# Kernel optimization log

Measured on AMD Instinct MI355X. Metric: run time of the kernel, lower is better.

Reference implementation:

```python
import jax, jax.numpy as jnp
import numpy as np

N, DIN, DOUT = 8192, 256, 128
NEG_SLOPE = 0.01         # F.leaky_relu default
MASK_VAL = -9.0e15       # from the torch source


def setup_inputs() -> dict:
    key = jax.random.key(0)
    kx, kadj, kW, kbW, ka1, ka2, kba = jax.random.split(key, 7)
    x = jax.random.normal(kx, (N, DIN), dtype=jnp.float32)
    adj = jax.random.randint(kadj, (N, N), 0, 2, dtype=jnp.int32)
    # Linear W: input_dim -> output_dim
    W = jax.random.normal(kW, (DIN, DOUT), dtype=jnp.float32) * (1.0 / np.sqrt(DIN))
    bW = jax.random.normal(kbW, (DOUT,), dtype=jnp.float32) * 0.01
    # Linear a: 2*output_dim -> 1, split into the h_i part (a1) and h_j part (a2)
    a1 = jax.random.normal(ka1, (DOUT,), dtype=jnp.float32) * (1.0 / np.sqrt(2 * DOUT))
    a2 = jax.random.normal(ka2, (DOUT,), dtype=jnp.float32) * (1.0 / np.sqrt(2 * DOUT))
    ba = jax.random.normal(kba, (), dtype=jnp.float32) * 0.01
    return {"x": x, "adj": adj, "W": W, "bW": bW, "a1": a1, "a2": a2, "ba": ba}


def reference(x, adj, W, bW, a1, a2, ba):
    # h = W x + b  -> [N, DOUT]
    h = x @ W + bW
    # e[i,j] = leaky_relu(a . [h_i, h_j] + ba) = leaky_relu(a1.h_i + a2.h_j + ba)
    s_src = h @ a1            # [N]
    s_dst = h @ a2            # [N]
    e = s_src[:, None] + s_dst[None, :] + ba   # [N, N]
    e = jnp.where(e > 0, e, NEG_SLOPE * e)
    # mask non-edges, row softmax over neighbors j
    e = jnp.where(adj > 0, e, MASK_VAL)
    alpha = jax.nn.softmax(e, axis=1)          # [N, N]
    # dropout is identity in eval mode (dropout_rate=0)
    return alpha @ h                            # [N, DOUT]
```

## Files before the change

kernel.cpp:

```cpp
#include <hip/hip_runtime.h>
#include <hip/hip_bf16.h>


#define NN 8192
#define DIN 256
#define DOUT 128
#define LOG2E 1.4426950408889634f

typedef __attribute__((ext_vector_type(8))) short short8;
typedef __attribute__((ext_vector_type(4))) float floatx4;

__global__ void prep_wt(const float* __restrict__ W, __hip_bfloat16* __restrict__ WT) {
    int e = blockIdx.x * blockDim.x + threadIdx.x;
    if (e < DIN * DOUT) {
        int k = e >> 7;
        int d = e & 127;
        WT[d * DIN + k] = __float2bfloat16(W[e]);
    }
}

__global__ __launch_bounds__(256, 4) void gat_h(
    const float* __restrict__ x, const __hip_bfloat16* __restrict__ WT,
    const float* __restrict__ bW, const float* __restrict__ a1, const float* __restrict__ a2,
    __hip_bfloat16* __restrict__ hbB, float* __restrict__ s_src, float* __restrict__ s_dst) {
    int tid = threadIdx.x;
    int w = tid >> 6, lane = tid & 63;
    int lm = lane & 15, lq = lane >> 4;
    int i0 = blockIdx.x * 32;
    int r0 = (w >> 1) * 16;
    int c0 = (w & 1) * 64;

    __shared__ float s1s[32], s2s[32];
    if (tid < 32) { s1s[tid] = 0.f; s2s[tid] = 0.f; }
    __syncthreads();

    floatx4 acc[4] = {};
#pragma unroll
    for (int kk = 0; kk < DIN; kk += 32) {
        const float4* xp = (const float4*)&x[(size_t)(i0 + r0 + lm) * DIN + kk + lq * 8];
        float4 xa = xp[0], xb = xp[1];
        union { short8 v; __hip_bfloat16 h[8]; } af;
        af.h[0] = __float2bfloat16(xa.x); af.h[1] = __float2bfloat16(xa.y);
        af.h[2] = __float2bfloat16(xa.z); af.h[3] = __float2bfloat16(xa.w);
        af.h[4] = __float2bfloat16(xb.x); af.h[5] = __float2bfloat16(xb.y);
        af.h[6] = __float2bfloat16(xb.z); af.h[7] = __float2bfloat16(xb.w);
#pragma unroll
        for (int t = 0; t < 4; t++) {
            int d = c0 + 16 * t + lm;
            short8 bf = *(const short8*)&WT[(size_t)d * DIN + kk + lq * 8];
            acc[t] = __builtin_amdgcn_mfma_f32_16x16x32_bf16(af.v, bf, acc[t], 0, 0, 0);
        }
    }
    float s1[4] = {0.f, 0.f, 0.f, 0.f}, s2[4] = {0.f, 0.f, 0.f, 0.f};
#pragma unroll
    for (int t = 0; t < 4; t++) {
        int d = c0 + 16 * t + lm;
        int f = (c0 >> 4) + t;
        float A1 = a1[d], A2 = a2[d], B = bW[d];
#pragma unroll
        for (int r = 0; r < 4; r++) {
            int k = r0 + lq * 4 + r;
            float h = acc[t][r] + B;
            hbB[(size_t)blockIdx.x * 4096 + f * 512 + (k >> 3) * 128 + lm * 8 + (k & 7)] =
                __float2bfloat16(h);
            s1[r] += h * A1;
            s2[r] += h * A2;
        }
    }
#pragma unroll
    for (int r = 0; r < 4; r++) {
        for (int m = 1; m < 16; m <<= 1) {
            s1[r] += __shfl_xor(s1[r], m, 64);
            s2[r] += __shfl_xor(s2[r], m, 64);
        }
    }
    if (lm == 0) {
#pragma unroll
        for (int r = 0; r < 4; r++) {
            int row = r0 + lq * 4 + r;
            atomicAdd(&s1s[row], s1[r]);
            atomicAdd(&s2s[row], s2[r]);
        }
    }
    __syncthreads();
    if (tid < 32) {
        s_src[i0 + tid] = s1s[tid] * LOG2E;
        s_dst[i0 + tid] = s2s[tid] * LOG2E;
    }
}

template <int NJT>
__global__ void build_mask(const int* __restrict__ adj, unsigned char* __restrict__ mask) {
    size_t gid = (size_t)blockIdx.x * blockDim.x + threadIdx.x;
    const int4* a = (const int4*)(adj + gid * 8);
    int4 v0 = a[0], v1 = a[1];
    unsigned int b = 0;
    b |= (v0.x != 0) ? 1u : 0u;
    b |= (v0.y != 0) ? 2u : 0u;
    b |= (v0.z != 0) ? 4u : 0u;
    b |= (v0.w != 0) ? 8u : 0u;
    b |= (v1.x != 0) ? 16u : 0u;
    b |= (v1.y != 0) ? 32u : 0u;
    b |= (v1.z != 0) ? 64u : 0u;
    b |= (v1.w != 0) ? 128u : 0u;
    unsigned int g = (unsigned int)gid & (NJT * 4 - 1);
    size_t pos = (gid & ~(size_t)(NJT * 4 - 1)) | ((g & 3) * NJT + (g >> 2));
    mask[pos] = (unsigned char)b;
}

__device__ inline short8 make_pfrag(unsigned int cm, float ssi, float4 cd0, float4 cd1,
                                    floatx4* accd, const short8 ones) {
    float p[8];
    float e;
    e = ssi + cd0.x; e = fmaxf(e, 0.01f * e); p[0] = (cm & 1u)   ? __builtin_amdgcn_exp2f(e) : 0.f;
    e = ssi + cd0.y; e = fmaxf(e, 0.01f * e); p[1] = (cm & 2u)   ? __builtin_amdgcn_exp2f(e) : 0.f;
    e = ssi + cd0.z; e = fmaxf(e, 0.01f * e); p[2] = (cm & 4u)   ? __builtin_amdgcn_exp2f(e) : 0.f;
    e = ssi + cd0.w; e = fmaxf(e, 0.01f * e); p[3] = (cm & 8u)   ? __builtin_amdgcn_exp2f(e) : 0.f;
    e = ssi + cd1.x; e = fmaxf(e, 0.01f * e); p[4] = (cm & 16u)  ? __builtin_amdgcn_exp2f(e) : 0.f;
    e = ssi + cd1.y; e = fmaxf(e, 0.01f * e); p[5] = (cm & 32u)  ? __builtin_amdgcn_exp2f(e) : 0.f;
    e = ssi + cd1.z; e = fmaxf(e, 0.01f * e); p[6] = (cm & 64u)  ? __builtin_amdgcn_exp2f(e) : 0.f;
    e = ssi + cd1.w; e = fmaxf(e, 0.01f * e); p[7] = (cm & 128u) ? __builtin_amdgcn_exp2f(e) : 0.f;
    union { short8 v; __hip_bfloat162 q[4]; } af;
    af.q[0] = __float22bfloat162_rn(make_float2(p[0], p[1]));
    af.q[1] = __float22bfloat162_rn(make_float2(p[2], p[3]));
    af.q[2] = __float22bfloat162_rn(make_float2(p[4], p[5]));
    af.q[3] = __float22bfloat162_rn(make_float2(p[6], p[7]));
    *accd = __builtin_amdgcn_mfma_f32_16x16x32_bf16(af.v, ones, *accd, 0, 0, 0);
    return af.v;
}

template <int NJT>
__global__ __launch_bounds__(256, 3) void gat_attn(
    const unsigned char* __restrict__ mask, const float* __restrict__ s_src,
    const float* __restrict__ s_dst, const float* __restrict__ ba_p,
    const __hip_bfloat16* __restrict__ hbB,
    float* __restrict__ num, float* __restrict__ lpart) {
    int tid = threadIdx.x;
    int w = tid >> 6, lane = tid & 63;
    int lm = lane & 15, lq = lane >> 4;
    int b = blockIdx.x;
    int ib = b & 63;
    int jh = b >> 6;
    int i0 = ib * 128 + w * 32;
    int jb0 = jh * (NJT * 32);

    const unsigned char* mrow0 = mask + (size_t)(i0 + lm) * (NN / 8) + jh * (NJT * 4) + lq * NJT;
    const unsigned char* mrow1 = mrow0 + (size_t)16 * (NN / 8);
    union Mr { uint4 v[NJT / 16]; unsigned int u[NJT / 4]; };
    Mr mr0, mr1;
#pragma unroll
    for (int q = 0; q < NJT / 16; q++) {
        mr0.v[q] = ((const uint4*)mrow0)[q];
        mr1.v[q] = ((const uint4*)mrow1)[q];
    }

    float ba = ba_p[0] * LOG2E;
    float ssi0 = s_src[i0 + lm] + ba;
    float ssi1 = s_src[i0 + 16 + lm] + ba;
    const float* sd = s_dst + jb0 + lq * 8;
    const __hip_bfloat16* hb = hbB + ((size_t)(jh * NJT) * 8) * 512 + lane * 8;

    floatx4 acc0[8] = {}, acc1[8] = {};
    floatx4 accd0 = {}, accd1 = {};
    const short8 ones = { 0x3F80, 0x3F80, 0x3F80, 0x3F80, 0x3F80, 0x3F80, 0x3F80, 0x3F80 };

#pragma unroll
    for (int t = 0; t < NJT; t++) {
        unsigned int cm0 = (mr0.u[t >> 2] >> ((t & 3) * 8)) & 0xFFu;
        unsigned int cm1 = (mr1.u[t >> 2] >> ((t & 3) * 8)) & 0xFFu;
        float4 cd0 = *(const float4*)(sd + t * 32);
        float4 cd1 = *(const float4*)(sd + t * 32 + 4);
        short8 af0 = make_pfrag(cm0, ssi0, cd0, cd1, &accd0, ones);
        short8 af1 = make_pfrag(cm1, ssi1, cd0, cd1, &accd1, ones);

        const __hip_bfloat16* hbt = hb + (size_t)t * 8 * 512;
#pragma unroll
        for (int f = 0; f < 8; f++) {
            short8 bf = *(const short8*)(hbt + f * 512);
            acc0[f] = __builtin_amdgcn_mfma_f32_16x16x32_bf16(af0, bf, acc0[f], 0, 0, 0);
            acc1[f] = __builtin_amdgcn_mfma_f32_16x16x32_bf16(af1, bf, acc1[f], 0, 0, 0);
        }
    }

    float* nb = num + ((size_t)jh * NN + i0) * DOUT;
#pragma unroll
    for (int f = 0; f < 8; f++)
#pragma unroll
        for (int r = 0; r < 4; r++) {
            nb[(size_t)(lq * 4 + r) * DOUT + f * 16 + lm] = acc0[f][r];
            nb[(size_t)(16 + lq * 4 + r) * DOUT + f * 16 + lm] = acc1[f][r];
        }
    if (lm == 0) {
#pragma unroll
        for (int r = 0; r < 4; r++) {
            lpart[(size_t)jh * NN + i0 + lq * 4 + r] = accd0[r];
            lpart[(size_t)jh * NN + i0 + 16 + lq * 4 + r] = accd1[r];
        }
    }
}

__global__ void gat_combine(const float* __restrict__ num, const float* __restrict__ lpart,
                            float* __restrict__ out, int jsplit) {
    int gid = blockIdx.x * blockDim.x + threadIdx.x;
    int idx = gid * 4;
    int i = idx >> 7;
    float den = 0.f;
    for (int s = 0; s < jsplit; s++) den += lpart[(size_t)s * NN + i];
    float inv = 1.0f / den;
    float4 o = make_float4(0.f, 0.f, 0.f, 0.f);
    for (int s = 0; s < jsplit; s++) {
        float4 n = *(const float4*)&num[(size_t)s * NN * DOUT + idx];
        o.x += n.x; o.y += n.y; o.z += n.z; o.w += n.w;
    }
    o.x *= inv; o.y *= inv; o.z *= inv; o.w *= inv;
    *(float4*)&out[idx] = o;
}

extern "C" void kernel_launch(void* const* d_in, const int* in_sizes, int n_in,
                              void* d_out, int out_size, void* d_ws, size_t ws_size,
                              hipStream_t stream) {
    const float* x  = (const float*)d_in[0];
    const int* adj  = (const int*)d_in[1];
    const float* W  = (const float*)d_in[2];
    const float* bW = (const float*)d_in[3];
    const float* a1 = (const float*)d_in[4];
    const float* a2 = (const float*)d_in[5];
    const float* ba = (const float*)d_in[6];
    float* out = (float*)d_out;

    char* ws = (char*)d_ws;
    __hip_bfloat16* hbB  = (__hip_bfloat16*)ws;
    __hip_bfloat16* WT   = (__hip_bfloat16*)(ws + 2097152);
    float* s_src         = (float*)(ws + 2162688);
    float* s_dst         = (float*)(ws + 2195456);
    float* lpart         = (float*)(ws + 2228224);
    unsigned char* mask  = (unsigned char*)(ws + 2752512);
    float* num           = (float*)(ws + 11141120);

    int jsplit = (ws_size >= 11141120 + (size_t)16 * NN * DOUT * 4) ? 16 : 8;

    if (jsplit == 16) build_mask<16><<<32768, 256, 0, stream>>>(adj, mask);
    else              build_mask<32><<<32768, 256, 0, stream>>>(adj, mask);
    prep_wt<<<128, 256, 0, stream>>>(W, WT);
    gat_h<<<256, 256, 0, stream>>>(x, WT, bW, a1, a2, hbB, s_src, s_dst);
    if (jsplit == 16)
        gat_attn<16><<<1024, 256, 0, stream>>>(mask, s_src, s_dst, ba, hbB, num, lpart);
    else
        gat_attn<32><<<512, 256, 0, stream>>>(mask, s_src, s_dst, ba, hbB, num, lpart);
    gat_combine<<<1024, 256, 0, stream>>>(num, lpart, out, jsplit);
}
```

Measured before the change: 437.3 us.

## Stream adjacency directly into LDS in attention kernel, drop mask-build pass

Removes the separate build_mask kernel, which read the full int32 adjacency and wrote a bit mask. The attention kernel now streams adjacency tiles straight into LDS with global_load_lds in a double buffer and reads the int values to decide masking. This saves one full pass over the 256 MB adjacency plus a kernel launch. In exchange it adds a __syncthreads per tile and 32 KB of LDS per block, which may reduce occupancy.

```diff
diff --git a/kernel.cpp b/kernel.cpp
--- a/kernel.cpp
+++ b/kernel.cpp
@@ -9,6 +9,8 @@
 
 typedef __attribute__((ext_vector_type(8))) short short8;
 typedef __attribute__((ext_vector_type(4))) float floatx4;
+typedef __attribute__((address_space(3))) void lds_void;
+typedef __attribute__((address_space(1))) void gbl_void;
 
 __global__ void prep_wt(const float* __restrict__ W, __hip_bfloat16* __restrict__ WT) {
     int e = blockIdx.x * blockDim.x + threadIdx.x;
@@ -89,37 +91,18 @@
     }
 }
 
-template <int NJT>
-__global__ void build_mask(const int* __restrict__ adj, unsigned char* __restrict__ mask) {
-    size_t gid = (size_t)blockIdx.x * blockDim.x + threadIdx.x;
-    const int4* a = (const int4*)(adj + gid * 8);
-    int4 v0 = a[0], v1 = a[1];
-    unsigned int b = 0;
-    b |= (v0.x != 0) ? 1u : 0u;
-    b |= (v0.y != 0) ? 2u : 0u;
-    b |= (v0.z != 0) ? 4u : 0u;
-    b |= (v0.w != 0) ? 8u : 0u;
-    b |= (v1.x != 0) ? 16u : 0u;
-    b |= (v1.y != 0) ? 32u : 0u;
-    b |= (v1.z != 0) ? 64u : 0u;
-    b |= (v1.w != 0) ? 128u : 0u;
-    unsigned int g = (unsigned int)gid & (NJT * 4 - 1);
-    size_t pos = (gid & ~(size_t)(NJT * 4 - 1)) | ((g & 3) * NJT + (g >> 2));
-    mask[pos] = (unsigned char)b;
-}
-
-__device__ inline short8 make_pfrag(unsigned int cm, float ssi, float4 cd0, float4 cd1,
+__device__ inline short8 make_pfrag(int4 m0, int4 m1, float ssi, float4 cd0, float4 cd1,
                                     floatx4* accd, const short8 ones) {
     float p[8];
     float e;
-    e = ssi + cd0.x; e = fmaxf(e, 0.01f * e); p[0] = (cm & 1u)   ? __builtin_amdgcn_exp2f(e) : 0.f;
-    e = ssi + cd0.y; e = fmaxf(e, 0.01f * e); p[1] = (cm & 2u)   ? __builtin_amdgcn_exp2f(e) : 0.f;
-    e = ssi + cd0.z; e = fmaxf(e, 0.01f * e); p[2] = (cm & 4u)   ? __builtin_amdgcn_exp2f(e) : 0.f;
-    e = ssi + cd0.w; e = fmaxf(e, 0.01f * e); p[3] = (cm & 8u)   ? __builtin_amdgcn_exp2f(e) : 0.f;
-    e = ssi + cd1.x; e = fmaxf(e, 0.01f * e); p[4] = (cm & 16u)  ? __builtin_amdgcn_exp2f(e) : 0.f;
-    e = ssi + cd1.y; e = fmaxf(e, 0.01f * e); p[5] = (cm & 32u)  ? __builtin_amdgcn_exp2f(e) : 0.f;
-    e = ssi + cd1.z; e = fmaxf(e, 0.01f * e); p[6] = (cm & 64u)  ? __builtin_amdgcn_exp2f(e) : 0.f;
-    e = ssi + cd1.w; e = fmaxf(e, 0.01f * e); p[7] = (cm & 128u) ? __builtin_amdgcn_exp2f(e) : 0.f;
+    e = ssi + cd0.x; e = fmaxf(e, 0.01f * e); p[0] = m0.x ? __builtin_amdgcn_exp2f(e) : 0.f;
+    e = ssi + cd0.y; e = fmaxf(e, 0.01f * e); p[1] = m0.y ? __builtin_amdgcn_exp2f(e) : 0.f;
+    e = ssi + cd0.z; e = fmaxf(e, 0.01f * e); p[2] = m0.z ? __builtin_amdgcn_exp2f(e) : 0.f;
+    e = ssi + cd0.w; e = fmaxf(e, 0.01f * e); p[3] = m0.w ? __builtin_amdgcn_exp2f(e) : 0.f;
+    e = ssi + cd1.x; e = fmaxf(e, 0.01f * e); p[4] = m1.x ? __builtin_amdgcn_exp2f(e) : 0.f;
+    e = ssi + cd1.y; e = fmaxf(e, 0.01f * e); p[5] = m1.y ? __builtin_amdgcn_exp2f(e) : 0.f;
+    e = ssi + cd1.z; e = fmaxf(e, 0.01f * e); p[6] = m1.z ? __builtin_amdgcn_exp2f(e) : 0.f;
+    e = ssi + cd1.w; e = fmaxf(e, 0.01f * e); p[7] = m1.w ? __builtin_amdgcn_exp2f(e) : 0.f;
     union { short8 v; __hip_bfloat162 q[4]; } af;
     af.q[0] = __float22bfloat162_rn(make_float2(p[0], p[1]));
     af.q[1] = __float22bfloat162_rn(make_float2(p[2], p[3]));
@@ -131,10 +114,11 @@
 
 template <int NJT>
 __global__ __launch_bounds__(256, 3) void gat_attn(
-    const unsigned char* __restrict__ mask, const float* __restrict__ s_src,
+    const int* __restrict__ adj, const float* __restrict__ s_src,
     const float* __restrict__ s_dst, const float* __restrict__ ba_p,
     const __hip_bfloat16* __restrict__ hbB,
     float* __restrict__ num, float* __restrict__ lpart) {
+    __shared__ int stg[2][4][1024];
     int tid = threadIdx.x;
     int w = tid >> 6, lane = tid & 63;
     int lm = lane & 15, lq = lane >> 4;
@@ -144,15 +128,7 @@
     int i0 = ib * 128 + w * 32;
     int jb0 = jh * (NJT * 32);
 
-    const unsigned char* mrow0 = mask + (size_t)(i0 + lm) * (NN / 8) + jh * (NJT * 4) + lq * NJT;
-    const unsigned char* mrow1 = mrow0 + (size_t)16 * (NN / 8);
-    union Mr { uint4 v[NJT / 16]; unsigned int u[NJT / 4]; };
-    Mr mr0, mr1;
-#pragma unroll
-    for (int q = 0; q < NJT / 16; q++) {
-        mr0.v[q] = ((const uint4*)mrow0)[q];
-        mr1.v[q] = ((const uint4*)mrow1)[q];
-    }
+    const int* gstage = adj + (size_t)(i0 + (lane >> 3)) * NN + jb0 + (lane & 7) * 4;
 
     float ba = ba_p[0] * LOG2E;
     float ssi0 = s_src[i0 + lm] + ba;
@@ -165,13 +141,30 @@
     const short8 ones = { 0x3F80, 0x3F80, 0x3F80, 0x3F80, 0x3F80, 0x3F80, 0x3F80, 0x3F80 };
 
 #pragma unroll
+    for (int q = 0; q < 4; q++)
+        __builtin_amdgcn_global_load_lds(
+            (const gbl_void*)(gstage + (size_t)q * 8 * NN),
+            (lds_void*)&stg[0][w][q * 256 + lane * 4], 16, 0, 0);
+
+#pragma unroll
     for (int t = 0; t < NJT; t++) {
-        unsigned int cm0 = (mr0.u[t >> 2] >> ((t & 3) * 8)) & 0xFFu;
-        unsigned int cm1 = (mr1.u[t >> 2] >> ((t & 3) * 8)) & 0xFFu;
+        __syncthreads();
+        if (t + 1 < NJT) {
+#pragma unroll
+            for (int q = 0; q < 4; q++)
+                __builtin_amdgcn_global_load_lds(
+                    (const gbl_void*)(gstage + (t + 1) * 32 + (size_t)q * 8 * NN),
+                    (lds_void*)&stg[(t + 1) & 1][w][q * 256 + lane * 4], 16, 0, 0);
+        }
+        const int* sb = &stg[t & 1][w][0];
+        int4 a00 = *(const int4*)&sb[lm * 32 + lq * 8];
+        int4 a01 = *(const int4*)&sb[lm * 32 + lq * 8 + 4];
+        int4 a10 = *(const int4*)&sb[(16 + lm) * 32 + lq * 8];
+        int4 a11 = *(const int4*)&sb[(16 + lm) * 32 + lq * 8 + 4];
         float4 cd0 = *(const float4*)(sd + t * 32);
         float4 cd1 = *(const float4*)(sd + t * 32 + 4);
-        short8 af0 = make_pfrag(cm0, ssi0, cd0, cd1, &accd0, ones);
-        short8 af1 = make_pfrag(cm1, ssi1, cd0, cd1, &accd1, ones);
+        short8 af0 = make_pfrag(a00, a01, ssi0, cd0, cd1, &accd0, ones);
+        short8 af1 = make_pfrag(a10, a11, ssi1, cd0, cd1, &accd1, ones);
 
         const __hip_bfloat16* hbt = hb + (size_t)t * 8 * 512;
 #pragma unroll
@@ -234,18 +227,15 @@
     float* s_src         = (float*)(ws + 2162688);
     float* s_dst         = (float*)(ws + 2195456);
     float* lpart         = (float*)(ws + 2228224);
-    unsigned char* mask  = (unsigned char*)(ws + 2752512);
-    float* num           = (float*)(ws + 11141120);
-
-    int jsplit = (ws_size >= 11141120 + (size_t)16 * NN * DOUT * 4) ? 16 : 8;
-
-    if (jsplit == 16) build_mask<16><<<32768, 256, 0, stream>>>(adj, mask);
-    else              build_mask<32><<<32768, 256, 0, stream>>>(adj, mask);
+    float* num           = (float*)(ws + 2752512);
+
+    int jsplit = (ws_size >= 2752512 + (size_t)16 * NN * DOUT * 4) ? 16 : 8;
+
     prep_wt<<<128, 256, 0, stream>>>(W, WT);
     gat_h<<<256, 256, 0, stream>>>(x, WT, bW, a1, a2, hbB, s_src, s_dst);
     if (jsplit == 16)
-        gat_attn<16><<<1024, 256, 0, stream>>>(mask, s_src, s_dst, ba, hbB, num, lpart);
+        gat_attn<16><<<1024, 256, 0, stream>>>(adj, s_src, s_dst, ba, hbB, num, lpart);
     else
-        gat_attn<32><<<512, 256, 0, stream>>>(mask, s_src, s_dst, ba, hbB, num, lpart);
+        gat_attn<32><<<512, 256, 0, stream>>>(adj, s_src, s_dst, ba, hbB, num, lpart);
     gat_combine<<<1024, 256, 0, stream>>>(num, lpart, out, jsplit);
 }
```

Result: slower. 453.2 us (+3.7%).

## Fuse split-K combine into attention kernel with per-block shared-memory reduction

Applied to the files above, without the earlier changes.

Each block now handles 32 rows across all columns, with its four waves splitting the column range and reducing numerators and denominators through shared-memory atomics. The normalization is done in-kernel, which removes the partial num/lpart buffers and the separate combine kernel. This removes a large round trip of partial results through global memory. In exchange, the grid shrinks to 256 blocks at low occupancy, and each block streams all of h, which raises L2 traffic and reduces latency hiding.

```diff
diff --git a/kernel.cpp b/kernel.cpp
--- a/kernel.cpp
+++ b/kernel.cpp
@@ -89,7 +89,6 @@
     }
 }
 
-template <int NJT>
 __global__ void build_mask(const int* __restrict__ adj, unsigned char* __restrict__ mask) {
     size_t gid = (size_t)blockIdx.x * blockDim.x + threadIdx.x;
     const int4* a = (const int4*)(adj + gid * 8);
@@ -103,8 +102,8 @@
     b |= (v1.y != 0) ? 32u : 0u;
     b |= (v1.z != 0) ? 64u : 0u;
     b |= (v1.w != 0) ? 128u : 0u;
-    unsigned int g = (unsigned int)gid & (NJT * 4 - 1);
-    size_t pos = (gid & ~(size_t)(NJT * 4 - 1)) | ((g & 3) * NJT + (g >> 2));
+    unsigned int g = (unsigned int)gid & 255u;
+    size_t pos = (gid & ~(size_t)255) | ((g & 3u) * 64u + (g >> 2));
     mask[pos] = (unsigned char)b;
 }
 
@@ -129,27 +128,26 @@
     return af.v;
 }
 
-template <int NJT>
-__global__ __launch_bounds__(256, 3) void gat_attn(
+__global__ __launch_bounds__(256, 1) void gat_attn(
     const unsigned char* __restrict__ mask, const float* __restrict__ s_src,
     const float* __restrict__ s_dst, const float* __restrict__ ba_p,
-    const __hip_bfloat16* __restrict__ hbB,
-    float* __restrict__ num, float* __restrict__ lpart) {
+    const __hip_bfloat16* __restrict__ hbB, float* __restrict__ out) {
+    __shared__ float red[32][128];
+    __shared__ float den[32];
     int tid = threadIdx.x;
     int w = tid >> 6, lane = tid & 63;
     int lm = lane & 15, lq = lane >> 4;
-    int b = blockIdx.x;
-    int ib = b & 63;
-    int jh = b >> 6;
-    int i0 = ib * 128 + w * 32;
-    int jb0 = jh * (NJT * 32);
-
-    const unsigned char* mrow0 = mask + (size_t)(i0 + lm) * (NN / 8) + jh * (NJT * 4) + lq * NJT;
+    int i0 = blockIdx.x * 32;
+
+    for (int q = tid; q < 32 * 128; q += 256) ((float*)red)[q] = 0.f;
+    if (tid < 32) den[tid] = 0.f;
+
+    const unsigned char* mrow0 = mask + (size_t)(i0 + lm) * (NN / 8) + w * 256 + lq * 64;
     const unsigned char* mrow1 = mrow0 + (size_t)16 * (NN / 8);
-    union Mr { uint4 v[NJT / 16]; unsigned int u[NJT / 4]; };
+    union Mr { uint4 v[4]; unsigned int u[16]; };
     Mr mr0, mr1;
 #pragma unroll
-    for (int q = 0; q < NJT / 16; q++) {
+    for (int q = 0; q < 4; q++) {
         mr0.v[q] = ((const uint4*)mrow0)[q];
         mr1.v[q] = ((const uint4*)mrow1)[q];
     }
@@ -157,15 +155,17 @@
     float ba = ba_p[0] * LOG2E;
     float ssi0 = s_src[i0 + lm] + ba;
     float ssi1 = s_src[i0 + 16 + lm] + ba;
-    const float* sd = s_dst + jb0 + lq * 8;
-    const __hip_bfloat16* hb = hbB + ((size_t)(jh * NJT) * 8) * 512 + lane * 8;
+    const float* sd = s_dst + w * 2048 + lq * 8;
+    const __hip_bfloat16* hb = hbB + (size_t)(w * 64) * 4096 + lane * 8;
 
     floatx4 acc0[8] = {}, acc1[8] = {};
     floatx4 accd0 = {}, accd1 = {};
     const short8 ones = { 0x3F80, 0x3F80, 0x3F80, 0x3F80, 0x3F80, 0x3F80, 0x3F80, 0x3F80 };
 
-#pragma unroll
-    for (int t = 0; t < NJT; t++) {
+    __syncthreads();
+
+#pragma unroll 4
+    for (int t = 0; t < 64; t++) {
         unsigned int cm0 = (mr0.u[t >> 2] >> ((t & 3) * 8)) & 0xFFu;
         unsigned int cm1 = (mr1.u[t >> 2] >> ((t & 3) * 8)) & 0xFFu;
         float4 cd0 = *(const float4*)(sd + t * 32);
@@ -173,7 +173,7 @@
         short8 af0 = make_pfrag(cm0, ssi0, cd0, cd1, &accd0, ones);
         short8 af1 = make_pfrag(cm1, ssi1, cd0, cd1, &accd1, ones);
 
-        const __hip_bfloat16* hbt = hb + (size_t)t * 8 * 512;
+        const __hip_bfloat16* hbt = hb + (size_t)t * 4096;
 #pragma unroll
         for (int f = 0; f < 8; f++) {
             short8 bf = *(const short8*)(hbt + f * 512);
@@ -182,38 +182,31 @@
         }
     }
 
-    float* nb = num + ((size_t)jh * NN + i0) * DOUT;
 #pragma unroll
     for (int f = 0; f < 8; f++)
 #pragma unroll
         for (int r = 0; r < 4; r++) {
-            nb[(size_t)(lq * 4 + r) * DOUT + f * 16 + lm] = acc0[f][r];
-            nb[(size_t)(16 + lq * 4 + r) * DOUT + f * 16 + lm] = acc1[f][r];
+            atomicAdd(&red[lq * 4 + r][f * 16 + lm], acc0[f][r]);
+            atomicAdd(&red[16 + lq * 4 + r][f * 16 + lm], acc1[f][r]);
         }
     if (lm == 0) {
 #pragma unroll
         for (int r = 0; r < 4; r++) {
-            lpart[(size_t)jh * NN + i0 + lq * 4 + r] = accd0[r];
-            lpart[(size_t)jh * NN + i0 + 16 + lq * 4 + r] = accd1[r];
-        }
-    }
-}
-
-__global__ void gat_combine(const float* __restrict__ num, const float* __restrict__ lpart,
-                            float* __restrict__ out, int jsplit) {
-    int gid = blockIdx.x * blockDim.x + threadIdx.x;
-    int idx = gid * 4;
-    int i = idx >> 7;
-    float den = 0.f;
-    for (int s = 0; s < jsplit; s++) den += lpart[(size_t)s * NN + i];
-    float inv = 1.0f / den;
-    float4 o = make_float4(0.f, 0.f, 0.f, 0.f);
-    for (int s = 0; s < jsplit; s++) {
-        float4 n = *(const float4*)&num[(size_t)s * NN * DOUT + idx];
-        o.x += n.x; o.y += n.y; o.z += n.z; o.w += n.w;
-    }
-    o.x *= inv; o.y *= inv; o.z *= inv; o.w *= inv;
-    *(float4*)&out[idx] = o;
+            atomicAdd(&den[lq * 4 + r], accd0[r]);
+            atomicAdd(&den[16 + lq * 4 + r], accd1[r]);
+        }
+    }
+    __syncthreads();
+
+    int row = tid >> 3, cb = (tid & 7) * 16;
+    float inv = 1.0f / den[row];
+    float* op = out + (size_t)(i0 + row) * DOUT + cb;
+#pragma unroll
+    for (int c = 0; c < 4; c++) {
+        float4 v = *(const float4*)&red[row][cb + c * 4];
+        v.x *= inv; v.y *= inv; v.z *= inv; v.w *= inv;
+        *(float4*)(op + c * 4) = v;
+    }
 }
 
 extern "C" void kernel_launch(void* const* d_in, const int* in_sizes, int n_in,
@@ -233,19 +226,10 @@
     __hip_bfloat16* WT   = (__hip_bfloat16*)(ws + 2097152);
     float* s_src         = (float*)(ws + 2162688);
     float* s_dst         = (float*)(ws + 2195456);
-    float* lpart         = (float*)(ws + 2228224);
-    unsigned char* mask  = (unsigned char*)(ws + 2752512);
-    float* num           = (float*)(ws + 11141120);
-
-    int jsplit = (ws_size >= 11141120 + (size_t)16 * NN * DOUT * 4) ? 16 : 8;
-
-    if (jsplit == 16) build_mask<16><<<32768, 256, 0, stream>>>(adj, mask);
-    else              build_mask<32><<<32768, 256, 0, stream>>>(adj, mask);
+    unsigned char* mask  = (unsigned char*)(ws + 2228224);
+
+    build_mask<<<32768, 256, 0, stream>>>(adj, mask);
     prep_wt<<<128, 256, 0, stream>>>(W, WT);
     gat_h<<<256, 256, 0, stream>>>(x, WT, bW, a1, a2, hbB, s_src, s_dst);
-    if (jsplit == 16)
-        gat_attn<16><<<1024, 256, 0, stream>>>(mask, s_src, s_dst, ba, hbB, num, lpart);
-    else
-        gat_attn<32><<<512, 256, 0, stream>>>(mask, s_src, s_dst, ba, hbB, num, lpart);
-    gat_combine<<<1024, 256, 0, stream>>>(num, lpart, out, jsplit);
-}
+    gat_attn<<<256, 256, 0, stream>>>(mask, s_src, s_dst, ba, hbB, out);
+}
```

Result: slower. 555.7 us (+27.1%).
